# Kernel tuning notes

Measured on AMD Instinct MI355X. Metric: run time of the kernel, lower is better.

Reference implementation:

```python
import jax, jax.numpy as jnp
import numpy as np
from jax import lax

B, H, W, C = 64, 224, 224, 3
FLAT = 27040  # 52*52*10 after localization convs/pools


def conv_relu(x, w, b):
    y = lax.conv_general_dilated(x, w, (1, 1), 'VALID',
                                 dimension_numbers=('NHWC', 'HWIO', 'NHWC'))
    return jax.nn.relu(y + b)


def maxpool2(x):
    return lax.reduce_window(x, -jnp.inf, lax.max, (1, 2, 2, 1), (1, 2, 2, 1), 'VALID')


def affine_grid(h, w, theta):
    # normalized coords in [-1, 1]
    xt, yt = jnp.meshgrid(jnp.linspace(-1.0, 1.0, w), jnp.linspace(-1.0, 1.0, h))
    grid = jnp.stack([xt.ravel(), yt.ravel(), jnp.ones(h * w, theta.dtype)], 0)  # (3, h*w)
    g = jnp.einsum('bij,jp->bip', theta, grid)  # (B, 2, h*w)
    return g.reshape(-1, 2, h, w)


def bilinear_sampler(img, xs, ys):
    # xs, ys: (B, h, w) in [-1, 1]; img: (B, H, W, C)
    max_y, max_x = img.shape[1] - 1, img.shape[2] - 1
    x = 0.5 * (xs + 1.0) * max_x
    y = 0.5 * (ys + 1.0) * max_y
    x0 = jnp.clip(jnp.floor(x).astype(jnp.int32), 0, max_x)
    x1 = jnp.clip(x0 + 1, 0, max_x)
    y0 = jnp.clip(jnp.floor(y).astype(jnp.int32), 0, max_y)
    y1 = jnp.clip(y0 + 1, 0, max_y)
    b = jnp.arange(img.shape[0])[:, None, None]
    Ia = img[b, y0, x0]  # (B,h,w,C)
    Ib = img[b, y1, x0]
    Ic = img[b, y0, x1]
    Id = img[b, y1, x1]
    x0f, x1f = x0.astype(x.dtype), x1.astype(x.dtype)
    y0f, y1f = y0.astype(y.dtype), y1.astype(y.dtype)
    wa = ((x1f - x) * (y1f - y))[..., None]
    wb = ((x1f - x) * (y - y0f))[..., None]
    wc = ((x - x0f) * (y1f - y))[..., None]
    wd = ((x - x0f) * (y - y0f))[..., None]
    return wa * Ia + wb * Ib + wc * Ic + wd * Id


def setup_inputs() -> dict:
    key = jax.random.key(0)
    ks = jax.random.split(key, 6)
    inputs = jax.random.normal(ks[0], (B, H, W, C), jnp.float32)
    conv1_w = jax.random.normal(ks[1], (7, 7, 3, 8), jnp.float32) * (2.0 / (7 * 7 * 3)) ** 0.5
    conv1_b = jnp.zeros((8,), jnp.float32)
    conv2_w = jax.random.normal(ks[2], (5, 5, 8, 10), jnp.float32) * (2.0 / (5 * 5 * 8)) ** 0.5
    conv2_b = jnp.zeros((10,), jnp.float32)
    fc1_w = jax.random.normal(ks[3], (FLAT, 32), jnp.float32) * (2.0 / FLAT) ** 0.5
    fc1_b = jnp.zeros((32,), jnp.float32)
    fc2_w = jax.random.normal(ks[4], (32, 6), jnp.float32) * 0.01
    fc2_b = jnp.array([1, 0, 0, 0, 1, 0], jnp.float32)  # identity affine init
    return dict(inputs=inputs, conv1_w=conv1_w, conv1_b=conv1_b,
                conv2_w=conv2_w, conv2_b=conv2_b, fc1_w=fc1_w, fc1_b=fc1_b,
                fc2_w=fc2_w, fc2_b=fc2_b)


def reference(inputs, conv1_w, conv1_b, conv2_w, conv2_b, fc1_w, fc1_b, fc2_w, fc2_b):
    xs = maxpool2(conv_relu(inputs, conv1_w, conv1_b))
    xs = maxpool2(conv_relu(xs, conv2_w, conv2_b))
    xs = xs.reshape(xs.shape[0], -1)  # (B, 27040)
    h1 = jax.nn.relu(xs @ fc1_w + fc1_b)
    theta = (h1 @ fc2_w + fc2_b).reshape(-1, 2, 3)
    grid = affine_grid(H, W, theta)  # (B, 2, H, W)
    return bilinear_sampler(inputs, grid[:, 0], grid[:, 1])
```

## Files before the change

### kernel.cpp

```cpp
#include <hip/hip_runtime.h>


__global__ __launch_bounds__(256) void k_wcvt(
    const float* __restrict__ w1, const float* __restrict__ b1,
    const float* __restrict__ w2, const float* __restrict__ b2,
    double* __restrict__ wd) {
  int t = blockIdx.x * 256 + threadIdx.x;
  if (t < 1176) wd[t] = (double)w1[t];
  else if (t < 1184) wd[t] = (double)b1[t - 1176];
  else if (t < 3184) wd[t] = (double)w2[t - 1184];
  else if (t < 3194) wd[t] = (double)b2[t - 3184];
}

__global__ __launch_bounds__(448) void k_conv1(
    const float* __restrict__ in, const double* __restrict__ wd,
    double* __restrict__ out) {
  __shared__ float win[14 * 672];

  int g = blockIdx.x & 7;
  int i = blockIdx.x >> 3;
  int b = g * 8 + i / 28;
  int tile = i % 28;
  int py0 = 4 * tile;
  int r0 = 8 * tile;

  {
    const float* ibb = in + (size_t)b * 150528;
    for (int idx = threadIdx.x; idx < 14 * 168; idx += 448) {
      int rr = idx / 168, c4 = idx % 168;
      int row = min(r0 + rr, 223);
      float4 v = reinterpret_cast<const float4*>(ibb + (size_t)row * 672)[c4];
      reinterpret_cast<float4*>(&win[rr * 672])[c4] = v;
    }
  }
  __syncthreads();

  int t = threadIdx.x;
  int py = py0 + t / 109;
  if (t < 436 && py < 109) {
    int px = t % 109;
    int lrb = 2 * (t / 109);

    double acc[2][2][8];
#pragma unroll
    for (int ii = 0; ii < 2; ++ii)
#pragma unroll
      for (int j = 0; j < 2; ++j)
#pragma unroll
        for (int k = 0; k < 8; ++k) acc[ii][j][k] = 0.0;

    for (int ky = 0; ky < 7; ++ky) {
      const float* r0p = &win[(lrb + ky) * 672 + 6 * px];
      const float* r1p = r0p + 672;
      float a0[24], a1[24];
#pragma unroll
      for (int j = 0; j < 12; ++j) {
        float2 u = reinterpret_cast<const float2*>(r0p)[j];
        a0[2 * j] = u.x; a0[2 * j + 1] = u.y;
        float2 v = reinterpret_cast<const float2*>(r1p)[j];
        a1[2 * j] = v.x; a1[2 * j + 1] = v.y;
      }
      const double* wk = wd + ky * 168;
#pragma unroll
      for (int kx = 0; kx < 7; ++kx) {
#pragma unroll
        for (int c = 0; c < 3; ++c) {
          double v00 = (double)a0[kx * 3 + c];
          double v01 = (double)a0[kx * 3 + 3 + c];
          double v10 = (double)a1[kx * 3 + c];
          double v11 = (double)a1[kx * 3 + 3 + c];
          const double* wp = wk + (kx * 3 + c) * 8;
#pragma unroll
          for (int oc = 0; oc < 8; ++oc) {
            double wv = wp[oc];
            acc[0][0][oc] = fma(v00, wv, acc[0][0][oc]);
            acc[0][1][oc] = fma(v01, wv, acc[0][1][oc]);
            acc[1][0][oc] = fma(v10, wv, acc[1][0][oc]);
            acc[1][1][oc] = fma(v11, wv, acc[1][1][oc]);
          }
        }
      }
    }

    double* op = out + ((size_t)b * 11881 + (size_t)py * 109 + px) * 8;
#pragma unroll
    for (int oc = 0; oc < 8; ++oc) {
      double m = fmax(fmax(acc[0][0][oc], acc[0][1][oc]),
                      fmax(acc[1][0][oc], acc[1][1][oc]));
      op[oc] = fmax(m + wd[1176 + oc], 0.0);
    }
  }
}

__global__ __launch_bounds__(512) void k_conv2(
    const double* __restrict__ in, const double* __restrict__ wd2,
    double* __restrict__ out) {
  __shared__ double win2[4 * 12 * 2 * 56];

  int g = blockIdx.x & 7;
  int i = blockIdx.x >> 3;
  int b = g * 8 + i / 13;
  int tile = i % 13;
  int py0 = 4 * tile;
  int r0 = 8 * tile;

  int t = threadIdx.x;
  int oh = __builtin_amdgcn_readfirstlane(t >> 8);
  int p = t & 255;
  bool valid = p < 208;
  int px = p % 52;
  int lrb = 2 * (p / 52);

  const double* wb = wd2 + oh * 5;

  double acc[2][2][5];
#pragma unroll
  for (int ii = 0; ii < 2; ++ii)
#pragma unroll
    for (int jj = 0; jj < 2; ++jj)
#pragma unroll
      for (int k = 0; k < 5; ++k) acc[ii][jj][k] = 0.0;

  const double* ib = in + (size_t)b * 11881 * 8;

  for (int h = 0; h < 2; ++h) {
    __syncthreads();
    for (int idx = threadIdx.x; idx < 12 * 109 * 2; idx += 512) {
      int d2 = idx & 1;
      int x  = (idx >> 1) % 109;
      int rr = (idx >> 1) / 109;
      double2 v = *reinterpret_cast<const double2*>(
          ib + ((size_t)(r0 + rr) * 109 + x) * 8 + h * 4 + d2 * 2);
      int par = x & 1, k = x >> 1;
      win2[(((d2 * 2) * 12 + rr) * 2 + par) * 56 + k] = v.x;
      win2[(((d2 * 2 + 1) * 12 + rr) * 2 + par) * 56 + k] = v.y;
    }
    __syncthreads();

    if (valid) {
#pragma unroll
      for (int ky = 0; ky < 5; ++ky) {
        int rr0 = lrb + ky;
#pragma unroll
        for (int cc = 0; cc < 4; ++cc) {
          int c = h * 4 + cc;
          const double* pe0 = &win2[((cc * 12 + rr0) * 2 + 0) * 56 + px];
          const double* po0 = &win2[((cc * 12 + rr0) * 2 + 1) * 56 + px];
          const double* pe1 = pe0 + 112;
          const double* po1 = po0 + 112;
          double e0[3] = {pe0[0], pe0[1], pe0[2]};
          double o0[3] = {po0[0], po0[1], po0[2]};
          double e1[3] = {pe1[0], pe1[1], pe1[2]};
          double o1[3] = {po1[0], po1[1], po1[2]};
#pragma unroll
          for (int kx = 0; kx < 5; ++kx) {
            double v00, v01, v10, v11;
            if (kx & 1) {
              v00 = o0[kx >> 1]; v01 = e0[(kx >> 1) + 1];
              v10 = o1[kx >> 1]; v11 = e1[(kx >> 1) + 1];
            } else {
              v00 = e0[kx >> 1]; v01 = o0[kx >> 1];
              v10 = e1[kx >> 1]; v11 = o1[kx >> 1];
            }
            const double* wp = wb + ((ky * 5 + kx) * 8 + c) * 10;
#pragma unroll
            for (int oc = 0; oc < 5; ++oc) {
              double wv = wp[oc];
              acc[0][0][oc] = fma(v00, wv, acc[0][0][oc]);
              acc[0][1][oc] = fma(v01, wv, acc[0][1][oc]);
              acc[1][0][oc] = fma(v10, wv, acc[1][0][oc]);
              acc[1][1][oc] = fma(v11, wv, acc[1][1][oc]);
            }
          }
        }
      }
    }
  }

  if (valid) {
    int pix = py0 * 52 + p;
    double* op = out + ((size_t)b * 2704 + pix) * 10 + oh * 5;
#pragma unroll
    for (int oc = 0; oc < 5; ++oc) {
      double m = fmax(fmax(acc[0][0][oc], acc[0][1][oc]),
                      fmax(acc[1][0][oc], acc[1][1][oc]));
      op[oc] = fmax(m + wd2[2000 + oh * 5 + oc], 0.0);
    }
  }
}

__global__ __launch_bounds__(256) void k_fc1(
    const double* __restrict__ xs, const float* __restrict__ w1,
    double* __restrict__ part) {
  int b = blockIdx.x >> 4;
  int q = blockIdx.x & 15;
  int oc = threadIdx.x & 31;
  int s = threadIdx.x >> 5;
  const double* xrow = xs + (size_t)b * 27040;

  int i0 = q * 1690 + s * 212;
  int i1 = min(i0 + 212, q * 1690 + 1690);
  double s0 = 0.0, s1 = 0.0;
  for (int i = i0; i + 1 < i1; i += 2) {
    s0 = fma(xrow[i],     (double)w1[(size_t)i * 32 + oc],       s0);
    s1 = fma(xrow[i + 1], (double)w1[(size_t)(i + 1) * 32 + oc], s1);
  }
  if ((i1 - i0) & 1)
    s0 = fma(xrow[i1 - 1], (double)w1[(size_t)(i1 - 1) * 32 + oc], s0);

  __shared__ double red[8][32];
  red[s][oc] = s0 + s1;
  __syncthreads();
  if (threadIdx.x < 32) {
    double v = 0.0;
#pragma unroll
    for (int k = 0; k < 8; ++k) v += red[k][threadIdx.x];
    part[((size_t)b * 16 + q) * 32 + threadIdx.x] = v;
  }
}

__global__ __launch_bounds__(64) void k_fc2(
    const double* __restrict__ part, const float* __restrict__ b1,
    const float* __restrict__ w2, const float* __restrict__ b2,
    double* __restrict__ theta) {
  int b = blockIdx.x;
  __shared__ double h1[32];
  if (threadIdx.x < 32) {
    double v = (double)b1[threadIdx.x];
#pragma unroll
    for (int q = 0; q < 16; ++q)
      v += part[((size_t)b * 16 + q) * 32 + threadIdx.x];
    h1[threadIdx.x] = v > 0.0 ? v : 0.0;
  }
  __syncthreads();
  if (threadIdx.x < 6) {
    double v = (double)b2[threadIdx.x];
#pragma unroll
    for (int k = 0; k < 32; ++k) v += h1[k] * (double)w2[k * 6 + threadIdx.x];
    theta[b * 6 + threadIdx.x] = v;
  }
}

__global__ __launch_bounds__(256) void k_sample(
    const float* __restrict__ img, const double* __restrict__ theta,
    float* __restrict__ out) {
  int idx = blockIdx.x * 256 + threadIdx.x;
  if (idx >= 64 * 224 * 224) return;
  int x = idx % 224;
  int t = idx / 224;
  int y = t % 224;
  int b = t / 224;

  const double* th = theta + b * 6;
  double t0 = th[0], t1 = th[1], t2 = th[2];
  double t3 = th[3], t4 = th[4], t5 = th[5];

  double xn = -1.0 + x * (2.0 / 223.0);
  double yn = -1.0 + y * (2.0 / 223.0);
  double xf = 0.5 * (t0 * xn + t1 * yn + t2 + 1.0) * 223.0;
  double yf = 0.5 * (t3 * xn + t4 * yn + t5 + 1.0) * 223.0;

  int x0 = (int)floor(xf);
  int y0 = (int)floor(yf);
  x0 = min(max(x0, 0), 223);
  y0 = min(max(y0, 0), 223);
  int x1 = min(x0 + 1, 223);
  int y1 = min(y0 + 1, 223);

  double x0f = (double)x0, x1f = (double)x1;
  double y0f = (double)y0, y1f = (double)y1;
  double wa = (x1f - xf) * (y1f - yf);
  double wb = (x1f - xf) * (yf - y0f);
  double wc = (xf - x0f) * (y1f - yf);
  double wd = (xf - x0f) * (yf - y0f);

  const float* p = img + (size_t)b * 150528;
  const float* Ia = p + ((size_t)y0 * 224 + x0) * 3;
  const float* Ib = p + ((size_t)y1 * 224 + x0) * 3;
  const float* Ic = p + ((size_t)y0 * 224 + x1) * 3;
  const float* Id = p + ((size_t)y1 * 224 + x1) * 3;

  float* op = out + (size_t)idx * 3;
#pragma unroll
  for (int c = 0; c < 3; ++c) {
    op[c] = (float)(wa * (double)Ia[c] + wb * (double)Ib[c] +
                    wc * (double)Ic[c] + wd * (double)Id[c]);
  }
}

extern "C" void kernel_launch(void* const* d_in, const int* in_sizes, int n_in,
                              void* d_out, int out_size, void* d_ws, size_t ws_size,
                              hipStream_t stream) {
  const float* inputs  = (const float*)d_in[0];
  const float* conv1_w = (const float*)d_in[1];
  const float* conv1_b = (const float*)d_in[2];
  const float* conv2_w = (const float*)d_in[3];
  const float* conv2_b = (const float*)d_in[4];
  const float* fc1_w   = (const float*)d_in[5];
  const float* fc1_b   = (const float*)d_in[6];
  const float* fc2_w   = (const float*)d_in[7];
  const float* fc2_b   = (const float*)d_in[8];
  float* outp = (float*)d_out;

  double* theta = (double*)d_ws;
  double* part  = (double*)((char*)d_ws + 4096);
  double* wd    = (double*)((char*)d_ws + 4096 + 262144);
  double* pool1 = (double*)((char*)d_ws + 4096 + 262144 + 25600);
  double* pool2 = pool1 + 6083072;

  k_wcvt<<<13, 256, 0, stream>>>(conv1_w, conv1_b, conv2_w, conv2_b, wd);
  k_conv1<<<28 * 64, 448, 0, stream>>>(inputs, wd, pool1);
  k_conv2<<<13 * 64, 512, 0, stream>>>(pool1, wd + 1184, pool2);
  k_fc1<<<1024, 256, 0, stream>>>(pool2, fc1_w, part);
  k_fc2<<<64, 64, 0, stream>>>(part, fc1_b, fc2_w, fc2_b, theta);
  k_sample<<<(64 * 224 * 224 + 255) / 256, 256, 0, stream>>>(inputs, theta, outp);
}
```

Baseline: 394.3 us.

## Store conv1 input window channel-planar with even/odd split and reuse rows across ky

The conv1 shared-memory window is reorganized into per-channel planes with even and odd x columns split, so each thread reads contiguous per-channel values at stride 1 across threads instead of stride 6. Input rows are held in a two-slot register ring, so each row loaded for the bottom pooling row is reused as the top row of the next ky iteration. Each float is converted to double once per channel rather than once per tap. The aim is fewer LDS loads and bank conflicts and fewer conversions, at the cost of a scattered scalar store pattern during the fill and a fully unrolled ky loop that raises register pressure.

```diff
diff --git a/kernel.cpp b/kernel.cpp
--- a/kernel.cpp
+++ b/kernel.cpp
@@ -15,7 +15,7 @@
 __global__ __launch_bounds__(448) void k_conv1(
     const float* __restrict__ in, const double* __restrict__ wd,
     double* __restrict__ out) {
-  __shared__ float win[14 * 672];
+  __shared__ float win[3 * 14 * 2 * 116];
 
   int g = blockIdx.x & 7;
   int i = blockIdx.x >> 3;
@@ -30,7 +30,14 @@
       int rr = idx / 168, c4 = idx % 168;
       int row = min(r0 + rr, 223);
       float4 v = reinterpret_cast<const float4*>(ibb + (size_t)row * 672)[c4];
-      reinterpret_cast<float4*>(&win[rr * 672])[c4] = v;
+      float vv[4] = {v.x, v.y, v.z, v.w};
+      int f0 = c4 * 4;
+#pragma unroll
+      for (int k = 0; k < 4; ++k) {
+        int f = f0 + k;
+        int c = f % 3, x = f / 3;
+        win[((c * 14 + rr) * 2 + (x & 1)) * 116 + (x >> 1)] = vv[k];
+      }
     }
   }
   __syncthreads();
@@ -49,26 +56,38 @@
 #pragma unroll
         for (int k = 0; k < 8; ++k) acc[ii][j][k] = 0.0;
 
+    float RB[2][3][8];
+    auto loadrow = [&](int rr, int pbuf) {
+#pragma unroll
+      for (int c = 0; c < 3; ++c) {
+        const float* pe = &win[((c * 14 + rr) * 2 + 0) * 116 + px];
+        const float* po = pe + 116;
+#pragma unroll
+        for (int k = 0; k < 4; ++k) {
+          RB[pbuf][c][2 * k]     = pe[k];
+          RB[pbuf][c][2 * k + 1] = po[k];
+        }
+      }
+    };
+    loadrow(lrb, 0);
+    loadrow(lrb + 1, 1);
+
+#pragma unroll
     for (int ky = 0; ky < 7; ++ky) {
-      const float* r0p = &win[(lrb + ky) * 672 + 6 * px];
-      const float* r1p = r0p + 672;
-      float a0[24], a1[24];
-#pragma unroll
-      for (int j = 0; j < 12; ++j) {
-        float2 u = reinterpret_cast<const float2*>(r0p)[j];
-        a0[2 * j] = u.x; a0[2 * j + 1] = u.y;
-        float2 v = reinterpret_cast<const float2*>(r1p)[j];
-        a1[2 * j] = v.x; a1[2 * j + 1] = v.y;
-      }
+      int top = ky & 1, bot = (ky + 1) & 1;
       const double* wk = wd + ky * 168;
 #pragma unroll
-      for (int kx = 0; kx < 7; ++kx) {
-#pragma unroll
-        for (int c = 0; c < 3; ++c) {
-          double v00 = (double)a0[kx * 3 + c];
-          double v01 = (double)a0[kx * 3 + 3 + c];
-          double v10 = (double)a1[kx * 3 + c];
-          double v11 = (double)a1[kx * 3 + 3 + c];
+      for (int c = 0; c < 3; ++c) {
+        double d0[8], d1[8];
+#pragma unroll
+        for (int j = 0; j < 8; ++j) {
+          d0[j] = (double)RB[top][c][j];
+          d1[j] = (double)RB[bot][c][j];
+        }
+#pragma unroll
+        for (int kx = 0; kx < 7; ++kx) {
+          double v00 = d0[kx], v01 = d0[kx + 1];
+          double v10 = d1[kx], v11 = d1[kx + 1];
           const double* wp = wk + (kx * 3 + c) * 8;
 #pragma unroll
           for (int oc = 0; oc < 8; ++oc) {
@@ -80,6 +99,7 @@
           }
         }
       }
+      if (ky < 6) loadrow(lrb + ky + 2, top);
     }
 
     double* op = out + ((size_t)b * 11881 + (size_t)py * 109 + px) * 8;
```

Result: slower. 406.0 us (+3.0%).

## Make conv1 persistent with register-staged double-buffered input tiles

Applied to the files above, without the earlier changes.

Conv1 now launches 256 blocks, and each block processes 7 consecutive row tiles instead of one. The next tile's input rows are prefetched into registers while the current tile is computed, then written to the alternate shared-memory buffer, hiding global load latency behind the FP64 FMA work. This doubles shared memory per block and adds registers for the staged float4s, which may lower occupancy. It also drops the old batch-interleaved block ordering.

```diff
diff --git a/kernel.cpp b/kernel.cpp
--- a/kernel.cpp
+++ b/kernel.cpp
@@ -15,80 +15,107 @@
 __global__ __launch_bounds__(448) void k_conv1(
     const float* __restrict__ in, const double* __restrict__ wd,
     double* __restrict__ out) {
-  __shared__ float win[14 * 672];
-
-  int g = blockIdx.x & 7;
-  int i = blockIdx.x >> 3;
-  int b = g * 8 + i / 28;
-  int tile = i % 28;
-  int py0 = 4 * tile;
-  int r0 = 8 * tile;
-
-  {
+  __shared__ float win[2][10260];
+
+  int t = threadIdx.x;
+  int px = t % 109;
+  int wrow = t / 109;
+  int lrb = 2 * wrow;
+
+  float4 st[6];
+  int gt0 = blockIdx.x * 7;
+
+  auto load_tile = [&](int gt) {
+    int b = gt / 28, tl = gt % 28;
+    int r0 = 8 * tl;
     const float* ibb = in + (size_t)b * 150528;
-    for (int idx = threadIdx.x; idx < 14 * 168; idx += 448) {
-      int rr = idx / 168, c4 = idx % 168;
-      int row = min(r0 + rr, 223);
-      float4 v = reinterpret_cast<const float4*>(ibb + (size_t)row * 672)[c4];
-      reinterpret_cast<float4*>(&win[rr * 672])[c4] = v;
-    }
-  }
+#pragma unroll
+    for (int r = 0; r < 6; ++r) {
+      int idx = t + r * 448;
+      if (idx < 2352) {
+        int rr = idx / 168, c4 = idx % 168;
+        int row = min(r0 + rr, 223);
+        st[r] = reinterpret_cast<const float4*>(ibb + (size_t)row * 672)[c4];
+      }
+    }
+  };
+  auto write_tile = [&](int buf) {
+#pragma unroll
+    for (int r = 0; r < 6; ++r) {
+      int idx = t + r * 448;
+      if (idx < 2352)
+        reinterpret_cast<float4*>(&win[buf][0])[idx] = st[r];
+    }
+  };
+
+  load_tile(gt0);
+  write_tile(0);
   __syncthreads();
 
-  int t = threadIdx.x;
-  int py = py0 + t / 109;
-  if (t < 436 && py < 109) {
-    int px = t % 109;
-    int lrb = 2 * (t / 109);
-
-    double acc[2][2][8];
-#pragma unroll
-    for (int ii = 0; ii < 2; ++ii)
-#pragma unroll
-      for (int j = 0; j < 2; ++j)
-#pragma unroll
-        for (int k = 0; k < 8; ++k) acc[ii][j][k] = 0.0;
-
-    for (int ky = 0; ky < 7; ++ky) {
-      const float* r0p = &win[(lrb + ky) * 672 + 6 * px];
-      const float* r1p = r0p + 672;
-      float a0[24], a1[24];
-#pragma unroll
-      for (int j = 0; j < 12; ++j) {
-        float2 u = reinterpret_cast<const float2*>(r0p)[j];
-        a0[2 * j] = u.x; a0[2 * j + 1] = u.y;
-        float2 v = reinterpret_cast<const float2*>(r1p)[j];
-        a1[2 * j] = v.x; a1[2 * j + 1] = v.y;
-      }
-      const double* wk = wd + ky * 168;
-#pragma unroll
-      for (int kx = 0; kx < 7; ++kx) {
-#pragma unroll
-        for (int c = 0; c < 3; ++c) {
-          double v00 = (double)a0[kx * 3 + c];
-          double v01 = (double)a0[kx * 3 + 3 + c];
-          double v10 = (double)a1[kx * 3 + c];
-          double v11 = (double)a1[kx * 3 + 3 + c];
-          const double* wp = wk + (kx * 3 + c) * 8;
-#pragma unroll
-          for (int oc = 0; oc < 8; ++oc) {
-            double wv = wp[oc];
-            acc[0][0][oc] = fma(v00, wv, acc[0][0][oc]);
-            acc[0][1][oc] = fma(v01, wv, acc[0][1][oc]);
-            acc[1][0][oc] = fma(v10, wv, acc[1][0][oc]);
-            acc[1][1][oc] = fma(v11, wv, acc[1][1][oc]);
+  for (int j = 0; j < 7; ++j) {
+    int gt = gt0 + j;
+    int b = gt / 28, tl = gt % 28;
+    int py0 = 4 * tl;
+    int cur = j & 1;
+
+    if (j < 6) load_tile(gt + 1);
+
+    int py = py0 + wrow;
+    if (t < 436 && py < 109) {
+      const float* wbuf = &win[cur][0];
+
+      double acc[2][2][8];
+#pragma unroll
+      for (int ii = 0; ii < 2; ++ii)
+#pragma unroll
+        for (int jj = 0; jj < 2; ++jj)
+#pragma unroll
+          for (int k = 0; k < 8; ++k) acc[ii][jj][k] = 0.0;
+
+      for (int ky = 0; ky < 7; ++ky) {
+        const float* r0p = &wbuf[(lrb + ky) * 672 + 6 * px];
+        const float* r1p = r0p + 672;
+        float a0[24], a1[24];
+#pragma unroll
+        for (int jj = 0; jj < 12; ++jj) {
+          float2 u = reinterpret_cast<const float2*>(r0p)[jj];
+          a0[2 * jj] = u.x; a0[2 * jj + 1] = u.y;
+          float2 v = reinterpret_cast<const float2*>(r1p)[jj];
+          a1[2 * jj] = v.x; a1[2 * jj + 1] = v.y;
+        }
+        const double* wk = wd + ky * 168;
+#pragma unroll
+        for (int kx = 0; kx < 7; ++kx) {
+#pragma unroll
+          for (int c = 0; c < 3; ++c) {
+            double v00 = (double)a0[kx * 3 + c];
+            double v01 = (double)a0[kx * 3 + 3 + c];
+            double v10 = (double)a1[kx * 3 + c];
+            double v11 = (double)a1[kx * 3 + 3 + c];
+            const double* wp = wk + (kx * 3 + c) * 8;
+#pragma unroll
+            for (int oc = 0; oc < 8; ++oc) {
+              double wv = wp[oc];
+              acc[0][0][oc] = fma(v00, wv, acc[0][0][oc]);
+              acc[0][1][oc] = fma(v01, wv, acc[0][1][oc]);
+              acc[1][0][oc] = fma(v10, wv, acc[1][0][oc]);
+              acc[1][1][oc] = fma(v11, wv, acc[1][1][oc]);
+            }
           }
         }
       }
-    }
-
-    double* op = out + ((size_t)b * 11881 + (size_t)py * 109 + px) * 8;
-#pragma unroll
-    for (int oc = 0; oc < 8; ++oc) {
-      double m = fmax(fmax(acc[0][0][oc], acc[0][1][oc]),
-                      fmax(acc[1][0][oc], acc[1][1][oc]));
-      op[oc] = fmax(m + wd[1176 + oc], 0.0);
-    }
+
+      double* op = out + ((size_t)b * 11881 + (size_t)py * 109 + px) * 8;
+#pragma unroll
+      for (int oc = 0; oc < 8; ++oc) {
+        double m = fmax(fmax(acc[0][0][oc], acc[0][1][oc]),
+                        fmax(acc[1][0][oc], acc[1][1][oc]));
+        op[oc] = fmax(m + wd[1176 + oc], 0.0);
+      }
+    }
+
+    if (j < 6) write_tile(cur ^ 1);
+    __syncthreads();
   }
 }
 
@@ -309,7 +336,7 @@
   double* pool2 = pool1 + 6083072;
 
   k_wcvt<<<13, 256, 0, stream>>>(conv1_w, conv1_b, conv2_w, conv2_b, wd);
-  k_conv1<<<28 * 64, 448, 0, stream>>>(inputs, wd, pool1);
+  k_conv1<<<256, 448, 0, stream>>>(inputs, wd, pool1);
   k_conv2<<<13 * 64, 512, 0, stream>>>(pool1, wd + 1184, pool2);
   k_fc1<<<1024, 256, 0, stream>>>(pool2, fc1_w, part);
   k_fc2<<<64, 64, 0, stream>>>(part, fc1_b, fc2_w, fc2_b, theta);
```

Result: slower. 456.3 us (+15.7%).

## Stage all conv2 input channels in shared memory once and reuse rows across ky

Applied to the files above, without the earlier changes.

The conv2 kernel now loads all 8 input channels of the window into shared memory in a single pass with one barrier, replacing two half-channel passes. The shared row stride is padded from 56 to 57 doubles to reduce bank conflicts. The loop order changes to channel-outer and ky-inner with a rolling two-row register buffer, so each shared row is read once rather than twice per ky step. The cost is more than double the shared memory per block (about 87 KB), which may lower occupancy.

```diff
diff --git a/kernel.cpp b/kernel.cpp
--- a/kernel.cpp
+++ b/kernel.cpp
@@ -95,7 +95,7 @@
 __global__ __launch_bounds__(512) void k_conv2(
     const double* __restrict__ in, const double* __restrict__ wd2,
     double* __restrict__ out) {
-  __shared__ double win2[4 * 12 * 2 * 56];
+  __shared__ double win2[8 * 12 * 2 * 57];
 
   int g = blockIdx.x & 7;
   int i = blockIdx.x >> 3;
@@ -112,6 +112,19 @@
   int lrb = 2 * (p / 52);
 
   const double* wb = wd2 + oh * 5;
+  const double* ib = in + (size_t)b * 11881 * 8;
+
+  for (int idx = threadIdx.x; idx < 12 * 109 * 4; idx += 512) {
+    int d2 = idx & 3;
+    int x  = (idx >> 2) % 109;
+    int rr = (idx >> 2) / 109;
+    double2 v = *reinterpret_cast<const double2*>(
+        ib + ((size_t)(r0 + rr) * 109 + x) * 8 + d2 * 2);
+    int par = x & 1, k = x >> 1;
+    win2[(((d2 * 2) * 12 + rr) * 2 + par) * 57 + k] = v.x;
+    win2[(((d2 * 2 + 1) * 12 + rr) * 2 + par) * 57 + k] = v.y;
+  }
+  __syncthreads();
 
   double acc[2][2][5];
 #pragma unroll
@@ -121,63 +134,48 @@
 #pragma unroll
       for (int k = 0; k < 5; ++k) acc[ii][jj][k] = 0.0;
 
-  const double* ib = in + (size_t)b * 11881 * 8;
-
-  for (int h = 0; h < 2; ++h) {
-    __syncthreads();
-    for (int idx = threadIdx.x; idx < 12 * 109 * 2; idx += 512) {
-      int d2 = idx & 1;
-      int x  = (idx >> 1) % 109;
-      int rr = (idx >> 1) / 109;
-      double2 v = *reinterpret_cast<const double2*>(
-          ib + ((size_t)(r0 + rr) * 109 + x) * 8 + h * 4 + d2 * 2);
-      int par = x & 1, k = x >> 1;
-      win2[(((d2 * 2) * 12 + rr) * 2 + par) * 56 + k] = v.x;
-      win2[(((d2 * 2 + 1) * 12 + rr) * 2 + par) * 56 + k] = v.y;
-    }
-    __syncthreads();
-
-    if (valid) {
+  if (valid) {
+#pragma unroll
+    for (int cc = 0; cc < 8; ++cc) {
+      double re[2][3], ro[2][3];
+      const double* cbase = &win2[(cc * 12) * 2 * 57 + px];
+#pragma unroll
+      for (int pb = 0; pb < 2; ++pb) {
+        const double* pe = cbase + (size_t)(lrb + pb) * 114;
+#pragma unroll
+        for (int k = 0; k < 3; ++k) { re[pb][k] = pe[k]; ro[pb][k] = pe[57 + k]; }
+      }
 #pragma unroll
       for (int ky = 0; ky < 5; ++ky) {
-        int rr0 = lrb + ky;
-#pragma unroll
-        for (int cc = 0; cc < 4; ++cc) {
-          int c = h * 4 + cc;
-          const double* pe0 = &win2[((cc * 12 + rr0) * 2 + 0) * 56 + px];
-          const double* po0 = &win2[((cc * 12 + rr0) * 2 + 1) * 56 + px];
-          const double* pe1 = pe0 + 112;
-          const double* po1 = po0 + 112;
-          double e0[3] = {pe0[0], pe0[1], pe0[2]};
-          double o0[3] = {po0[0], po0[1], po0[2]};
-          double e1[3] = {pe1[0], pe1[1], pe1[2]};
-          double o1[3] = {po1[0], po1[1], po1[2]};
-#pragma unroll
-          for (int kx = 0; kx < 5; ++kx) {
-            double v00, v01, v10, v11;
-            if (kx & 1) {
-              v00 = o0[kx >> 1]; v01 = e0[(kx >> 1) + 1];
-              v10 = o1[kx >> 1]; v11 = e1[(kx >> 1) + 1];
-            } else {
-              v00 = e0[kx >> 1]; v01 = o0[kx >> 1];
-              v10 = e1[kx >> 1]; v11 = o1[kx >> 1];
-            }
-            const double* wp = wb + ((ky * 5 + kx) * 8 + c) * 10;
-#pragma unroll
-            for (int oc = 0; oc < 5; ++oc) {
-              double wv = wp[oc];
-              acc[0][0][oc] = fma(v00, wv, acc[0][0][oc]);
-              acc[0][1][oc] = fma(v01, wv, acc[0][1][oc]);
-              acc[1][0][oc] = fma(v10, wv, acc[1][0][oc]);
-              acc[1][1][oc] = fma(v11, wv, acc[1][1][oc]);
-            }
+        int top = ky & 1, bot = (ky + 1) & 1;
+#pragma unroll
+        for (int kx = 0; kx < 5; ++kx) {
+          double v00, v01, v10, v11;
+          if (kx & 1) {
+            v00 = ro[top][kx >> 1]; v01 = re[top][(kx >> 1) + 1];
+            v10 = ro[bot][kx >> 1]; v11 = re[bot][(kx >> 1) + 1];
+          } else {
+            v00 = re[top][kx >> 1]; v01 = ro[top][kx >> 1];
+            v10 = re[bot][kx >> 1]; v11 = ro[bot][kx >> 1];
+          }
+          const double* wp = wb + ((ky * 5 + kx) * 8 + cc) * 10;
+#pragma unroll
+          for (int oc = 0; oc < 5; ++oc) {
+            double wv = wp[oc];
+            acc[0][0][oc] = fma(v00, wv, acc[0][0][oc]);
+            acc[0][1][oc] = fma(v01, wv, acc[0][1][oc]);
+            acc[1][0][oc] = fma(v10, wv, acc[1][0][oc]);
+            acc[1][1][oc] = fma(v11, wv, acc[1][1][oc]);
           }
         }
+        if (ky < 4) {
+          const double* pe = cbase + (size_t)(lrb + ky + 2) * 114;
+#pragma unroll
+          for (int k = 0; k < 3; ++k) { re[top][k] = pe[k]; ro[top][k] = pe[57 + k]; }
+        }
       }
     }
-  }
-
-  if (valid) {
+
     int pix = py0 * 52 + p;
     double* op = out + ((size_t)b * 2704 + pix) * 10 + oh * 5;
 #pragma unroll
```

Measured after the change: 407.2 us. +3.3%, slower.
